# Performance work log

Hardware: AMD Instinct MI355X
Metric: run time of the kernel (lower is better)

The kernel has to match this reference:

```python
import jax, jax.numpy as jnp
import numpy as np

# fixed geometry: N = B2D * H * W pixels
B2D, H, W = 32, 112, 112
NCLS, NSUB, DIM = 4, 2, 256
PROTO_MOM = 0.999
SK_ITERS, SK_EPS = 3, 0.05
LN_EPS = 1e-5


def layer_norm(x, gamma, beta):
    mu = jnp.mean(x, axis=-1, keepdims=True)
    var = jnp.var(x, axis=-1, keepdims=True)
    return (x - mu) * jax.lax.rsqrt(var + LN_EPS) * gamma + beta


def l2_normalize(x):
    return x / jnp.maximum(jnp.linalg.norm(x, axis=-1, keepdims=True), 1e-12)


def masked_sinkhorn(sim_c, mask):
    # sim_c: [N, M] cosine sims for one class; mask: [N] bool (pixels of this class)
    # Faithful to distributed_sinkhorn, restricted to masked rows.
    m = mask.astype(sim_c.dtype)
    L = jnp.exp(sim_c / SK_EPS).T * m[None, :]          # [M, N]
    Bn = jnp.sum(m)
    M = L.shape[0]
    L = L / jnp.maximum(jnp.sum(L), 1e-30)
    for _ in range(SK_ITERS):
        L = L / jnp.maximum(jnp.sum(L, axis=1, keepdims=True), 1e-30) / M
        col = jnp.sum(L, axis=0, keepdims=True)
        L = jnp.where(m[None, :] > 0, L / jnp.maximum(col, 1e-30) / jnp.maximum(Bn, 1.0), 0.0)
    L = (L * Bn).T                                       # [N, M]
    idx = jnp.argmax(L, axis=1)
    q = jax.nn.one_hot(idx, M, dtype=sim_c.dtype) * m[:, None]  # hard assignment
    return q, idx


def setup_inputs() -> dict:
    key = jax.random.key(0)
    ks = jax.random.split(key, 3)
    N = B2D * H * W
    return {
        "out_feat": jax.random.normal(ks[0], (N, DIM), dtype=jnp.float32),
        "label": jax.random.randint(ks[1], (N,), 0, NCLS, dtype=jnp.int64),
        "prototypes": jax.random.normal(ks[2], (NCLS, NSUB, DIM), dtype=jnp.float32),
        "fn_gamma": jnp.ones((DIM,), jnp.float32),
        "fn_beta": jnp.zeros((DIM,), jnp.float32),
        "mn_gamma": jnp.ones((NCLS,), jnp.float32),
        "mn_beta": jnp.zeros((NCLS,), jnp.float32),
    }


def reference(out_feat, label, prototypes, fn_gamma, fn_beta, mn_gamma, mn_beta):
    N = out_feat.shape[0]
    feat = l2_normalize(layer_norm(out_feat, fn_gamma, fn_beta))      # [N, D]
    protos = l2_normalize(prototypes)                                  # [K, M, D]
    sim = jnp.einsum('nd,kmd->nmk', feat, protos)                      # [N, M, K]
    nearest = layer_norm(jnp.max(sim, axis=1), mn_gamma, mn_beta)      # [N, K]
    pred = jnp.argmax(nearest, axis=-1)
    correct = (label == pred)                                          # [N] bool

    proto_logits = sim.reshape(N, NSUB * NCLS)
    proto_target = jnp.zeros((N,), jnp.float32)
    new_protos = protos
    for c in range(NCLS):
        cls_mask = (label == c)
        q, idx = masked_sinkhorn(sim[:, :, c], cls_mask)               # q:[N,M], masked
        mk = (cls_mask & correct).astype(feat.dtype)[:, None]
        m_q = q * mk                                                   # [N, M]
        f = m_q.T @ (feat * mk)                                        # [M, D]
        n = jnp.sum(m_q, axis=0)                                       # [M]
        f = l2_normalize(f)
        upd = PROTO_MOM * protos[c] + (1.0 - PROTO_MOM) * f
        upd = jnp.where(((jnp.sum(n) > 0) & (n != 0))[:, None], upd, protos[c])
        new_protos = new_protos.at[c].set(upd)
        proto_target = jnp.where(cls_mask, idx.astype(jnp.float32) + NSUB * c, proto_target)
    new_protos = l2_normalize(new_protos)

    nearest_img = nearest.reshape(B2D, H, W, NCLS).transpose(0, 3, 1, 2)  # [b, K, h, w]
    return nearest_img, proto_logits, proto_target, new_protos
```

## Files before the change

### kernel.cpp

```cpp
#include <hip/hip_runtime.h>
#include <stdint.h>

#define N_PIX 401408
#define HWIMG 12544
#define LN_EPS 1e-5f

struct Ws {
  double R[3][8];
  unsigned cnt4[4];
  unsigned nmk[8];
  float  protoN[8][256];
  float  fAcc[8][256];
  unsigned char flags[N_PIX];
};

__device__ __forceinline__ float wredf(float v) {
#pragma unroll
  for (int o = 32; o > 0; o >>= 1) v += __shfl_xor(v, o, 64);
  return v;
}
__device__ __forceinline__ float wred16(float v) {
  v += __shfl_xor(v, 1, 64);
  v += __shfl_xor(v, 2, 64);
  v += __shfl_xor(v, 4, 64);
  v += __shfl_xor(v, 8, 64);
  return v;
}
__device__ __forceinline__ double wredd(double v) {
#pragma unroll
  for (int o = 32; o > 0; o >>= 1) v += __shfl_xor(v, o, 64);
  return v;
}
__device__ __forceinline__ unsigned wredu(unsigned v) {
#pragma unroll
  for (int o = 32; o > 0; o >>= 1) v += (unsigned)__shfl_xor((int)v, o, 64);
  return v;
}

__global__ __launch_bounds__(256) void k_main(
    const float* __restrict__ X, const int* __restrict__ label,
    const float* __restrict__ protos,
    const float* __restrict__ fng, const float* __restrict__ fnb,
    const float* __restrict__ mng, const float* __restrict__ mnb,
    Ws* __restrict__ ws,
    float* __restrict__ out_nearest, float* __restrict__ out_logits) {
  __shared__ float prS[16 * 132];
  int tid = threadIdx.x;
  int wave = tid >> 6, lane = tid & 63;

  if (blockIdx.x == 0) {
    if (tid < 24) ((double*)ws->R)[tid] = 0.0;
    if (tid >= 24 && tid < 32) ws->nmk[tid - 24] = 0u;
    if (tid >= 32 && tid < 36) ws->cnt4[tid - 32] = 0u;
    for (int i = tid; i < 2048; i += 256) (&ws->fAcc[0][0])[i] = 0.f;
  }

#pragma unroll
  for (int t = 0; t < 2; t++) {
    int r = wave + t * 4;
    const float4 p = *(const float4*)(protos + r * 256 + lane * 4);
    float ss = p.x * p.x + p.y * p.y + p.z * p.z + p.w * p.w;
    ss = wredf(ss);
    float inv = 1.0f / fmaxf(sqrtf(ss), 1e-12f);
    float4 o; o.x = p.x * inv; o.y = p.y * inv; o.z = p.z * inv; o.w = p.w * inv;
    int sd = lane >> 2;
    *(float4*)(&prS[sd * 132 + r * 16 + (lane & 3) * 4]) = o;
    if (blockIdx.x == 0) *(float4*)(&ws->protoN[r][lane * 4]) = o;
  }
  __syncthreads();

  int grp = lane >> 4, s = lane & 15;
  int n = blockIdx.x * 16 + wave * 4 + grp;

  const float* xb = X + (size_t)n * 256 + s * 16;
  const float4 x0 = *(const float4*)(xb);
  const float4 x1 = *(const float4*)(xb + 4);
  const float4 x2 = *(const float4*)(xb + 8);
  const float4 x3 = *(const float4*)(xb + 12);
  int lab = label[n];

  float sm = (x0.x + x0.y + x0.z + x0.w) + (x1.x + x1.y + x1.z + x1.w) +
             (x2.x + x2.y + x2.z + x2.w) + (x3.x + x3.y + x3.z + x3.w);
  float q = x0.x * x0.x + x0.y * x0.y + x0.z * x0.z + x0.w * x0.w +
            x1.x * x1.x + x1.y * x1.y + x1.z * x1.z + x1.w * x1.w +
            x2.x * x2.x + x2.y * x2.y + x2.z * x2.z + x2.w * x2.w +
            x3.x * x3.x + x3.y * x3.y + x3.z * x3.z + x3.w * x3.w;
  sm = wred16(sm); q = wred16(q);
  float mu = sm * (1.0f / 256.0f);
  float var = q * (1.0f / 256.0f) - mu * mu;
  float rstd = rsqrtf(var + LN_EPS);

  const float* gb = fng + s * 16;
  const float* bb = fnb + s * 16;
  const float4 g0 = *(const float4*)(gb);
  const float4 g1 = *(const float4*)(gb + 4);
  const float4 g2 = *(const float4*)(gb + 8);
  const float4 g3 = *(const float4*)(gb + 12);
  const float4 b0 = *(const float4*)(bb);
  const float4 b1 = *(const float4*)(bb + 4);
  const float4 b2 = *(const float4*)(bb + 8);
  const float4 b3 = *(const float4*)(bb + 12);

  float4 y0, y1, y2, y3;
  y0.x = (x0.x - mu) * rstd * g0.x + b0.x; y0.y = (x0.y - mu) * rstd * g0.y + b0.y;
  y0.z = (x0.z - mu) * rstd * g0.z + b0.z; y0.w = (x0.w - mu) * rstd * g0.w + b0.w;
  y1.x = (x1.x - mu) * rstd * g1.x + b1.x; y1.y = (x1.y - mu) * rstd * g1.y + b1.y;
  y1.z = (x1.z - mu) * rstd * g1.z + b1.z; y1.w = (x1.w - mu) * rstd * g1.w + b1.w;
  y2.x = (x2.x - mu) * rstd * g2.x + b2.x; y2.y = (x2.y - mu) * rstd * g2.y + b2.y;
  y2.z = (x2.z - mu) * rstd * g2.z + b2.z; y2.w = (x2.w - mu) * rstd * g2.w + b2.w;
  y3.x = (x3.x - mu) * rstd * g3.x + b3.x; y3.y = (x3.y - mu) * rstd * g3.y + b3.y;
  y3.z = (x3.z - mu) * rstd * g3.z + b3.z; y3.w = (x3.w - mu) * rstd * g3.w + b3.w;

  float qq = y0.x * y0.x + y0.y * y0.y + y0.z * y0.z + y0.w * y0.w +
             y1.x * y1.x + y1.y * y1.y + y1.z * y1.z + y1.w * y1.w +
             y2.x * y2.x + y2.y * y2.y + y2.z * y2.z + y2.w * y2.w +
             y3.x * y3.x + y3.y * y3.y + y3.z * y3.z + y3.w * y3.w;
  qq = wred16(qq);

  float dot[8];
#pragma unroll
  for (int j = 0; j < 8; j++) {
    const float* pj = &prS[s * 132 + j * 16];
    const float4 pa = *(const float4*)(pj);
    const float4 pb = *(const float4*)(pj + 4);
    const float4 pc = *(const float4*)(pj + 8);
    const float4 pd = *(const float4*)(pj + 12);
    dot[j] = y0.x * pa.x + y0.y * pa.y + y0.z * pa.z + y0.w * pa.w +
             y1.x * pb.x + y1.y * pb.y + y1.z * pb.z + y1.w * pb.w +
             y2.x * pc.x + y2.y * pc.y + y2.z * pc.z + y2.w * pc.w +
             y3.x * pd.x + y3.y * pd.y + y3.z * pd.z + y3.w * pd.w;
  }
#pragma unroll
  for (int o = 1; o <= 4; o <<= 1) {
#pragma unroll
    for (int j = 0; j < 8; j++) dot[j] += __shfl_xor(dot[j], o, 64);
  }
  int bsel = s & 7;
  float t0 = (bsel & 1) ? dot[1] : dot[0];
  float t1 = (bsel & 1) ? dot[3] : dot[2];
  float t2 = (bsel & 1) ? dot[5] : dot[4];
  float t3 = (bsel & 1) ? dot[7] : dot[6];
  float u0 = (bsel & 2) ? t1 : t0;
  float u1v = (bsel & 2) ? t3 : t2;
  float v = (bsel & 4) ? u1v : u0;
  v += __shfl_xor(v, 8, 64);

  float inv = 1.0f / fmaxf(sqrtf(qq), 1e-12f);
  float d = v * inv;

  if (s < 8) out_logits[(size_t)n * 8 + ((s & 1) << 2) + (s >> 1)] = d;

  float nm = fmaxf(d, __shfl_xor(d, 1, 64));
  float tA = __shfl_xor(nm, 2, 64);
  float s2 = nm + tA, q2 = nm * nm + tA * tA;
  float s4 = s2 + __shfl_xor(s2, 4, 64);
  float q4 = q2 + __shfl_xor(q2, 4, 64);
  float m4 = 0.25f * s4;
  float v4 = 0.25f * q4 - m4 * m4;
  float rs4 = rsqrtf(v4 + LN_EPS);
  int k = (s >> 1) & 3;
  float lnv = (nm - m4) * rs4 * mng[k] + mnb[k];

  int bimg = n / HWIMG;
  int p = n - bimg * HWIMG;
  if (s < 8 && (s & 1) == 0)
    out_nearest[((size_t)bimg * 4 + k) * HWIMG + p] = lnv;

  float av = lnv; int ak = k;
#pragma unroll
  for (int o = 2; o <= 4; o <<= 1) {
    float ov = __shfl_xor(av, o, 64);
    int ok = __shfl_xor(ak, o, 64);
    bool take = (ov > av) || (ov == av && ok < ak);
    av = take ? ov : av;
    ak = take ? ok : ak;
  }
  if (s == 0) ws->flags[n] = (lab == ak) ? (unsigned char)1 : (unsigned char)0;
}

template <int ITER>
__global__ __launch_bounds__(256) void k_sink(const float* __restrict__ logits,
                                              const int* __restrict__ label,
                                              Ws* __restrict__ ws) {
  __shared__ float su1[8], su2[8], sBn[4];
  int tid = threadIdx.x;
  if (ITER >= 2) {
    if (tid < 8) {
      int c = tid >> 1;
      float S = (float)ws->R[0][c * 2] + (float)ws->R[0][c * 2 + 1];
      float uu0 = 1.0f / fmaxf(S, 1e-30f);
      float R0 = (float)ws->R[0][tid];
      float uu1 = uu0 / (fmaxf(uu0 * R0, 1e-30f) * 2.0f);
      su1[tid] = uu1;
      if (ITER >= 3) {
        float R1 = (float)ws->R[1][tid];
        su2[tid] = uu1 / (fmaxf(uu1 * R1, 1e-30f) * 2.0f);
      }
    }
    if (tid < 4) sBn[tid] = fmaxf((float)ws->cnt4[tid], 1.0f);
  }
  __syncthreads();

  double a0 = 0, a1 = 0, a2 = 0, a3 = 0, a4 = 0, a5 = 0, a6 = 0, a7 = 0;
  unsigned c0 = 0, c1 = 0, c2 = 0, c3 = 0;
  int gtid = blockIdx.x * 256 + tid;
  int T = gridDim.x * 256;
  for (int n = gtid; n < N_PIX; n += T) {
    int c = label[n];
    const float4 la = *(const float4*)(logits + (size_t)n * 8);
    const float4 lb = *(const float4*)(logits + (size_t)n * 8 + 4);
    float s0 = (c & 2) ? ((c & 1) ? la.w : la.z) : ((c & 1) ? la.y : la.x);
    float s1 = (c & 2) ? ((c & 1) ? lb.w : lb.z) : ((c & 1) ? lb.y : lb.x);
    float E0 = expf(s0 / 0.05f);
    float E1 = expf(s1 / 0.05f);
    float v = 1.0f;
    if (ITER >= 2) {
      float S1 = su1[c * 2] * E0 + su1[c * 2 + 1] * E1;
      float v1 = 1.0f / (fmaxf(S1, 1e-30f) * sBn[c]);
      v = v1;
      if (ITER >= 3) {
        float S2 = su2[c * 2] * E0 + su2[c * 2 + 1] * E1;
        v = v1 / (fmaxf(v1 * S2, 1e-30f) * sBn[c]);
      }
    }
    double t0 = (double)(v * E0), t1 = (double)(v * E1);
    if (c == 0) { a0 += t0; a1 += t1; c0++; }
    else if (c == 1) { a2 += t0; a3 += t1; c1++; }
    else if (c == 2) { a4 += t0; a5 += t1; c2++; }
    else { a6 += t0; a7 += t1; c3++; }
  }
  a0 = wredd(a0); a1 = wredd(a1); a2 = wredd(a2); a3 = wredd(a3);
  a4 = wredd(a4); a5 = wredd(a5); a6 = wredd(a6); a7 = wredd(a7);
  __shared__ double lds[4][8];
  __shared__ unsigned ldc[4][4];
  int wave = tid >> 6, lane = tid & 63;
  if (ITER == 1) { c0 = wredu(c0); c1 = wredu(c1); c2 = wredu(c2); c3 = wredu(c3); }
  if (lane == 0) {
    lds[wave][0] = a0; lds[wave][1] = a1; lds[wave][2] = a2; lds[wave][3] = a3;
    lds[wave][4] = a4; lds[wave][5] = a5; lds[wave][6] = a6; lds[wave][7] = a7;
    if (ITER == 1) { ldc[wave][0] = c0; ldc[wave][1] = c1; ldc[wave][2] = c2; ldc[wave][3] = c3; }
  }
  __syncthreads();
  if (tid < 8) {
    double ssum = lds[0][tid] + lds[1][tid] + lds[2][tid] + lds[3][tid];
    unsafeAtomicAdd(&ws->R[ITER - 1][tid], ssum);
  }
  if (ITER == 1 && tid < 4) {
    unsigned cs = ldc[0][tid] + ldc[1][tid] + ldc[2][tid] + ldc[3][tid];
    atomicAdd(&ws->cnt4[tid], cs);
  }
}

__global__ __launch_bounds__(256) void k_accum(
    const float* __restrict__ X, const int* __restrict__ label,
    const float* __restrict__ fng, const float* __restrict__ fnb,
    const float* __restrict__ logits, Ws* __restrict__ ws,
    float* __restrict__ out_target) {
  __shared__ float fa[4 * 2048];
  __shared__ float su[8];
  __shared__ unsigned ldc[4][8];
  int tid = threadIdx.x;
  if (tid < 8) {
    int c = tid >> 1;
    float S = (float)ws->R[0][c * 2] + (float)ws->R[0][c * 2 + 1];
    float uu0 = 1.0f / fmaxf(S, 1e-30f);
    float R0 = (float)ws->R[0][tid];
    float uu1 = uu0 / (fmaxf(uu0 * R0, 1e-30f) * 2.0f);
    float R1 = (float)ws->R[1][tid];
    float uu2 = uu1 / (fmaxf(uu1 * R1, 1e-30f) * 2.0f);
    float R2 = (float)ws->R[2][tid];
    su[tid] = uu2 / (fmaxf(uu2 * R2, 1e-30f) * 2.0f);
  }
  for (int i = tid; i < 4 * 2048; i += 256) fa[i] = 0.f;
  __syncthreads();

  int wave = tid >> 6, lane = tid & 63;
  const float4 g4 = *(const float4*)(fng + lane * 4);
  const float4 b4 = *(const float4*)(fnb + lane * 4);
  float* myAcc = &fa[wave * 2048];

  unsigned cl[8] = {0, 0, 0, 0, 0, 0, 0, 0};
  int gw = blockIdx.x * 4 + wave;
  int GW = gridDim.x * 4;
  for (int ch = gw; ch < N_PIX / 64; ch += GW) {
    int n = ch * 64 + lane;
    int c = label[n];
    int fl = ws->flags[n];
    float s0 = logits[(size_t)n * 8 + c];
    float s1 = logits[(size_t)n * 8 + 4 + c];
    float E0 = expf(s0 / 0.05f);
    float E1 = expf(s1 / 0.05f);
    int idx = (su[c * 2 + 1] * E1 > su[c * 2] * E0) ? 1 : 0;
    out_target[n] = (float)(idx + 2 * c);
    int bucket = c * 2 + idx;
#pragma unroll
    for (int j = 0; j < 8; j++) cl[j] += (fl && bucket == j) ? 1u : 0u;

    unsigned long long mask = __ballot(fl);
    while (mask) {
      int src = __builtin_ctzll(mask);
      mask &= (mask - 1);
      int cc = __shfl(c, src, 64);
      int ii = __shfl(idx, src, 64);
      int nn = ch * 64 + src;
      const float4 x = *(const float4*)(X + (size_t)nn * 256 + lane * 4);
      float s = x.x + x.y + x.z + x.w;
      float q = x.x * x.x + x.y * x.y + x.z * x.z + x.w * x.w;
      s = wredf(s); q = wredf(q);
      float mu = s * (1.0f / 256.0f);
      float var = q * (1.0f / 256.0f) - mu * mu;
      float rstd = rsqrtf(var + LN_EPS);
      float y0 = (x.x - mu) * rstd * g4.x + b4.x;
      float y1 = (x.y - mu) * rstd * g4.y + b4.y;
      float y2 = (x.z - mu) * rstd * g4.z + b4.z;
      float y3 = (x.w - mu) * rstd * g4.w + b4.w;
      float qq = y0 * y0 + y1 * y1 + y2 * y2 + y3 * y3;
      qq = wredf(qq);
      float inv = 1.0f / fmaxf(sqrtf(qq), 1e-12f);
      float* dst = myAcc + (cc * 2 + ii) * 256 + lane * 4;
      dst[0] += y0 * inv; dst[1] += y1 * inv; dst[2] += y2 * inv; dst[3] += y3 * inv;
    }
  }
#pragma unroll
  for (int j = 0; j < 8; j++) cl[j] = wredu(cl[j]);
  if (lane == 0) {
#pragma unroll
    for (int j = 0; j < 8; j++) ldc[wave][j] = cl[j];
  }
  __syncthreads();
  float* fg = &ws->fAcc[0][0];
  for (int i = tid; i < 2048; i += 256) {
    float ssum = fa[i] + fa[2048 + i] + fa[4096 + i] + fa[6144 + i];
    unsafeAtomicAdd(fg + i, ssum);
  }
  if (tid < 8) {
    unsigned cs = ldc[0][tid] + ldc[1][tid] + ldc[2][tid] + ldc[3][tid];
    if (cs) atomicAdd(&ws->nmk[tid], cs);
  }
}

__global__ __launch_bounds__(512) void k_final(Ws* __restrict__ ws, float* __restrict__ out_protos) {
  int tid = threadIdx.x;
  int r = tid >> 6, lane = tid & 63;
  const float4 f = *(const float4*)(&ws->fAcc[r][lane * 4]);
  float ss = wredf(f.x * f.x + f.y * f.y + f.z * f.z + f.w * f.w);
  float invf = 1.0f / fmaxf(sqrtf(ss), 1e-12f);
  unsigned nr = ws->nmk[r];
  int c = r >> 1;
  unsigned tot = ws->nmk[c * 2] + ws->nmk[c * 2 + 1];
  bool cond = (tot > 0u) && (nr != 0u);
  const float4 p = *(const float4*)(&ws->protoN[r][lane * 4]);
  float u0 = cond ? 0.999f * p.x + 0.001f * (f.x * invf) : p.x;
  float u1 = cond ? 0.999f * p.y + 0.001f * (f.y * invf) : p.y;
  float u2 = cond ? 0.999f * p.z + 0.001f * (f.z * invf) : p.z;
  float u3 = cond ? 0.999f * p.w + 0.001f * (f.w * invf) : p.w;
  float ss2 = wredf(u0 * u0 + u1 * u1 + u2 * u2 + u3 * u3);
  float invn = 1.0f / fmaxf(sqrtf(ss2), 1e-12f);
  float4 o; o.x = u0 * invn; o.y = u1 * invn; o.z = u2 * invn; o.w = u3 * invn;
  *(float4*)(out_protos + r * 256 + lane * 4) = o;
}

extern "C" void kernel_launch(void* const* d_in, const int* in_sizes, int n_in,
                              void* d_out, int out_size, void* d_ws, size_t ws_size,
                              hipStream_t stream) {
  const float* X = (const float*)d_in[0];
  const int* label = (const int*)d_in[1];
  const float* protos = (const float*)d_in[2];
  const float* fng = (const float*)d_in[3];
  const float* fnb = (const float*)d_in[4];
  const float* mng = (const float*)d_in[5];
  const float* mnb = (const float*)d_in[6];

  float* out = (float*)d_out;
  float* out_nearest = out;
  float* out_logits = out + 1605632;
  float* out_target = out_logits + 3211264;
  float* out_protos = out_target + N_PIX;
  Ws* ws = (Ws*)d_ws;

  k_main<<<N_PIX / 16, 256, 0, stream>>>(X, label, protos, fng, fnb, mng, mnb, ws, out_nearest, out_logits);
  k_sink<1><<<512, 256, 0, stream>>>(out_logits, label, ws);
  k_sink<2><<<512, 256, 0, stream>>>(out_logits, label, ws);
  k_sink<3><<<512, 256, 0, stream>>>(out_logits, label, ws);
  k_accum<<<512, 256, 0, stream>>>(X, label, fng, fnb, out_logits, ws, out_target);
  k_final<<<1, 512, 0, stream>>>(ws, out_protos);
}
```

Measured before the change: 670.3 us.

## Fuse first Sinkhorn pass into main kernel and pack per-pixel class sims

Moves prototype normalization into a separate init kernel. The main kernel now processes 256 pixels per block with 8 lanes per pixel and also computes the first Sinkhorn row sums and class counts, so the k_sink<1> launch is gone. It writes the two class-specific similarities into a compact ePack buffer, which the later Sinkhorn and accumulation passes read instead of the strided logits array. It adds a fast path that skips the gamma/beta multiply when they are identity, and doubles the accum grid. The costs are an extra kernel launch, more registers per thread, and a larger workspace.

```diff
diff --git a/kernel.cpp b/kernel.cpp
--- a/kernel.cpp
+++ b/kernel.cpp
@@ -11,6 +11,7 @@
   unsigned nmk[8];
   float  protoN[8][256];
   float  fAcc[8][256];
+  float  ePack[N_PIX][2];
   unsigned char flags[N_PIX];
 };
 
@@ -19,13 +20,6 @@
   for (int o = 32; o > 0; o >>= 1) v += __shfl_xor(v, o, 64);
   return v;
 }
-__device__ __forceinline__ float wred16(float v) {
-  v += __shfl_xor(v, 1, 64);
-  v += __shfl_xor(v, 2, 64);
-  v += __shfl_xor(v, 4, 64);
-  v += __shfl_xor(v, 8, 64);
-  return v;
-}
 __device__ __forceinline__ double wredd(double v) {
 #pragma unroll
   for (int o = 32; o > 0; o >>= 1) v += __shfl_xor(v, o, 64);
@@ -37,225 +31,274 @@
   return v;
 }
 
+__global__ __launch_bounds__(512) void k_init(const float* __restrict__ protos, Ws* __restrict__ ws) {
+  int tid = threadIdx.x;
+  if (tid < 24) ((double*)ws->R)[tid] = 0.0;
+  if (tid >= 24 && tid < 32) ws->nmk[tid - 24] = 0u;
+  if (tid >= 32 && tid < 36) ws->cnt4[tid - 32] = 0u;
+  float* fa = &ws->fAcc[0][0];
+  for (int i = tid; i < 8 * 256; i += 512) fa[i] = 0.f;
+
+  int r = tid >> 6, lane = tid & 63;
+  const float4 p = *(const float4*)(protos + r * 256 + lane * 4);
+  float ss = p.x * p.x + p.y * p.y + p.z * p.z + p.w * p.w;
+  ss = wredf(ss);
+  float inv = 1.0f / fmaxf(sqrtf(ss), 1e-12f);
+  float4 o; o.x = p.x * inv; o.y = p.y * inv; o.z = p.z * inv; o.w = p.w * inv;
+  *(float4*)(&ws->protoN[r][lane * 4]) = o;
+}
+
 __global__ __launch_bounds__(256) void k_main(
     const float* __restrict__ X, const int* __restrict__ label,
-    const float* __restrict__ protos,
     const float* __restrict__ fng, const float* __restrict__ fnb,
     const float* __restrict__ mng, const float* __restrict__ mnb,
     Ws* __restrict__ ws,
     float* __restrict__ out_nearest, float* __restrict__ out_logits) {
-  __shared__ float prS[16 * 132];
+  __shared__ float prS[8 * 260];
+  __shared__ double sR[4][8];
+  __shared__ unsigned sC[4][4];
   int tid = threadIdx.x;
   int wave = tid >> 6, lane = tid & 63;
-
-  if (blockIdx.x == 0) {
-    if (tid < 24) ((double*)ws->R)[tid] = 0.0;
-    if (tid >= 24 && tid < 32) ws->nmk[tid - 24] = 0u;
-    if (tid >= 32 && tid < 36) ws->cnt4[tid - 32] = 0u;
-    for (int i = tid; i < 2048; i += 256) (&ws->fAcc[0][0])[i] = 0.f;
-  }
-
-#pragma unroll
-  for (int t = 0; t < 2; t++) {
-    int r = wave + t * 4;
-    const float4 p = *(const float4*)(protos + r * 256 + lane * 4);
-    float ss = p.x * p.x + p.y * p.y + p.z * p.z + p.w * p.w;
-    ss = wredf(ss);
-    float inv = 1.0f / fmaxf(sqrtf(ss), 1e-12f);
-    float4 o; o.x = p.x * inv; o.y = p.y * inv; o.z = p.z * inv; o.w = p.w * inv;
-    int sd = lane >> 2;
-    *(float4*)(&prS[sd * 132 + r * 16 + (lane & 3) * 4]) = o;
-    if (blockIdx.x == 0) *(float4*)(&ws->protoN[r][lane * 4]) = o;
-  }
-  __syncthreads();
-
-  int grp = lane >> 4, s = lane & 15;
-  int n = blockIdx.x * 16 + wave * 4 + grp;
-
-  const float* xb = X + (size_t)n * 256 + s * 16;
-  const float4 x0 = *(const float4*)(xb);
-  const float4 x1 = *(const float4*)(xb + 4);
-  const float4 x2 = *(const float4*)(xb + 8);
-  const float4 x3 = *(const float4*)(xb + 12);
-  int lab = label[n];
-
-  float sm = (x0.x + x0.y + x0.z + x0.w) + (x1.x + x1.y + x1.z + x1.w) +
-             (x2.x + x2.y + x2.z + x2.w) + (x3.x + x3.y + x3.z + x3.w);
-  float q = x0.x * x0.x + x0.y * x0.y + x0.z * x0.z + x0.w * x0.w +
-            x1.x * x1.x + x1.y * x1.y + x1.z * x1.z + x1.w * x1.w +
-            x2.x * x2.x + x2.y * x2.y + x2.z * x2.z + x2.w * x2.w +
-            x3.x * x3.x + x3.y * x3.y + x3.z * x3.z + x3.w * x3.w;
-  sm = wred16(sm); q = wred16(q);
-  float mu = sm * (1.0f / 256.0f);
-  float var = q * (1.0f / 256.0f) - mu * mu;
-  float rstd = rsqrtf(var + LN_EPS);
-
-  const float* gb = fng + s * 16;
-  const float* bb = fnb + s * 16;
-  const float4 g0 = *(const float4*)(gb);
-  const float4 g1 = *(const float4*)(gb + 4);
-  const float4 g2 = *(const float4*)(gb + 8);
-  const float4 g3 = *(const float4*)(gb + 12);
-  const float4 b0 = *(const float4*)(bb);
-  const float4 b1 = *(const float4*)(bb + 4);
-  const float4 b2 = *(const float4*)(bb + 8);
-  const float4 b3 = *(const float4*)(bb + 12);
-
-  float4 y0, y1, y2, y3;
-  y0.x = (x0.x - mu) * rstd * g0.x + b0.x; y0.y = (x0.y - mu) * rstd * g0.y + b0.y;
-  y0.z = (x0.z - mu) * rstd * g0.z + b0.z; y0.w = (x0.w - mu) * rstd * g0.w + b0.w;
-  y1.x = (x1.x - mu) * rstd * g1.x + b1.x; y1.y = (x1.y - mu) * rstd * g1.y + b1.y;
-  y1.z = (x1.z - mu) * rstd * g1.z + b1.z; y1.w = (x1.w - mu) * rstd * g1.w + b1.w;
-  y2.x = (x2.x - mu) * rstd * g2.x + b2.x; y2.y = (x2.y - mu) * rstd * g2.y + b2.y;
-  y2.z = (x2.z - mu) * rstd * g2.z + b2.z; y2.w = (x2.w - mu) * rstd * g2.w + b2.w;
-  y3.x = (x3.x - mu) * rstd * g3.x + b3.x; y3.y = (x3.y - mu) * rstd * g3.y + b3.y;
-  y3.z = (x3.z - mu) * rstd * g3.z + b3.z; y3.w = (x3.w - mu) * rstd * g3.w + b3.w;
-
-  float qq = y0.x * y0.x + y0.y * y0.y + y0.z * y0.z + y0.w * y0.w +
-             y1.x * y1.x + y1.y * y1.y + y1.z * y1.z + y1.w * y1.w +
-             y2.x * y2.x + y2.y * y2.y + y2.z * y2.z + y2.w * y2.w +
-             y3.x * y3.x + y3.y * y3.y + y3.z * y3.z + y3.w * y3.w;
-  qq = wred16(qq);
-
-  float dot[8];
-#pragma unroll
-  for (int j = 0; j < 8; j++) {
-    const float* pj = &prS[s * 132 + j * 16];
-    const float4 pa = *(const float4*)(pj);
-    const float4 pb = *(const float4*)(pj + 4);
-    const float4 pc = *(const float4*)(pj + 8);
-    const float4 pd = *(const float4*)(pj + 12);
-    dot[j] = y0.x * pa.x + y0.y * pa.y + y0.z * pa.z + y0.w * pa.w +
-             y1.x * pb.x + y1.y * pb.y + y1.z * pb.z + y1.w * pb.w +
-             y2.x * pc.x + y2.y * pc.y + y2.z * pc.z + y2.w * pc.w +
-             y3.x * pd.x + y3.y * pd.y + y3.z * pd.z + y3.w * pd.w;
-  }
-#pragma unroll
-  for (int o = 1; o <= 4; o <<= 1) {
-#pragma unroll
-    for (int j = 0; j < 8; j++) dot[j] += __shfl_xor(dot[j], o, 64);
-  }
-  int bsel = s & 7;
-  float t0 = (bsel & 1) ? dot[1] : dot[0];
-  float t1 = (bsel & 1) ? dot[3] : dot[2];
-  float t2 = (bsel & 1) ? dot[5] : dot[4];
-  float t3 = (bsel & 1) ? dot[7] : dot[6];
-  float u0 = (bsel & 2) ? t1 : t0;
-  float u1v = (bsel & 2) ? t3 : t2;
-  float v = (bsel & 4) ? u1v : u0;
-  v += __shfl_xor(v, 8, 64);
-
-  float inv = 1.0f / fmaxf(sqrtf(qq), 1e-12f);
-  float d = v * inv;
-
-  if (s < 8) out_logits[(size_t)n * 8 + ((s & 1) << 2) + (s >> 1)] = d;
-
-  float nm = fmaxf(d, __shfl_xor(d, 1, 64));
-  float tA = __shfl_xor(nm, 2, 64);
-  float s2 = nm + tA, q2 = nm * nm + tA * tA;
-  float s4 = s2 + __shfl_xor(s2, 4, 64);
-  float q4 = q2 + __shfl_xor(q2, 4, 64);
-  float m4 = 0.25f * s4;
-  float v4 = 0.25f * q4 - m4 * m4;
-  float rs4 = rsqrtf(v4 + LN_EPS);
-  int k = (s >> 1) & 3;
-  float lnv = (nm - m4) * rs4 * mng[k] + mnb[k];
-
-  int bimg = n / HWIMG;
-  int p = n - bimg * HWIMG;
-  if (s < 8 && (s & 1) == 0)
-    out_nearest[((size_t)bimg * 4 + k) * HWIMG + p] = lnv;
-
-  float av = lnv; int ak = k;
-#pragma unroll
-  for (int o = 2; o <= 4; o <<= 1) {
-    float ov = __shfl_xor(av, o, 64);
-    int ok = __shfl_xor(ak, o, 64);
-    bool take = (ov > av) || (ov == av && ok < ak);
-    av = take ? ov : av;
-    ak = take ? ok : ak;
-  }
-  if (s == 0) ws->flags[n] = (lab == ak) ? (unsigned char)1 : (unsigned char)0;
+  int s = lane & 7, g = lane >> 3;
+
+  {
+    int ps = tid >> 5, pj = (tid >> 2) & 7, ph = tid & 3;
+    const float* src = &ws->protoN[pj][ps * 32 + ph * 8];
+    float4 a = *(const float4*)src;
+    float4 b = *(const float4*)(src + 4);
+    float* dst = &prS[ps * 260 + pj * 32 + ph * 8];
+    *(float4*)dst = a;
+    *(float4*)(dst + 4) = b;
+  }
+
+  bool triv;
+  {
+    bool ok = true;
+    const float* gp = fng + s * 32;
+    const float* bp = fnb + s * 32;
+#pragma unroll
+    for (int q = 0; q < 8; q++) {
+      float4 gq = *(const float4*)(gp + q * 4);
+      float4 bq = *(const float4*)(bp + q * 4);
+      ok = ok && gq.x == 1.f && gq.y == 1.f && gq.z == 1.f && gq.w == 1.f &&
+           bq.x == 0.f && bq.y == 0.f && bq.z == 0.f && bq.w == 0.f;
+    }
+    triv = (bool)__all(ok);
+  }
+  float mngk = mng[s >> 1], mnbk = mnb[s >> 1];
+  __syncthreads();
+
+  double eAcc = 0.0;
+  unsigned cAcc = 0u;
+
+  const int base = blockIdx.x * 256;
+#pragma unroll 1
+  for (int it = 0; it < 8; ++it) {
+    int n = base + it * 32 + wave * 8 + g;
+    const float* xb = X + (size_t)n * 256 + s * 32;
+    float4 Y[8];
+#pragma unroll
+    for (int q = 0; q < 8; q++) Y[q] = *(const float4*)(xb + q * 4);
+    int lab = label[n];
+
+    float sm = 0.f, sq = 0.f;
+#pragma unroll
+    for (int q = 0; q < 8; q++) {
+      sm += Y[q].x + Y[q].y + Y[q].z + Y[q].w;
+      sq += Y[q].x * Y[q].x + Y[q].y * Y[q].y + Y[q].z * Y[q].z + Y[q].w * Y[q].w;
+    }
+    sm += __shfl_xor(sm, 1, 64); sq += __shfl_xor(sq, 1, 64);
+    sm += __shfl_xor(sm, 2, 64); sq += __shfl_xor(sq, 2, 64);
+    sm += __shfl_xor(sm, 4, 64); sq += __shfl_xor(sq, 4, 64);
+    float mu = sm * (1.0f / 256.0f);
+    float var = sq * (1.0f / 256.0f) - mu * mu;
+    float rstd = rsqrtf(var + LN_EPS);
+
+    if (triv) {
+#pragma unroll
+      for (int q = 0; q < 8; q++) {
+        Y[q].x = (Y[q].x - mu) * rstd; Y[q].y = (Y[q].y - mu) * rstd;
+        Y[q].z = (Y[q].z - mu) * rstd; Y[q].w = (Y[q].w - mu) * rstd;
+      }
+    } else {
+      const float* gp = fng + s * 32;
+      const float* bp = fnb + s * 32;
+#pragma unroll
+      for (int q = 0; q < 8; q++) {
+        float4 gq = *(const float4*)(gp + q * 4);
+        float4 bq = *(const float4*)(bp + q * 4);
+        Y[q].x = (Y[q].x - mu) * rstd * gq.x + bq.x;
+        Y[q].y = (Y[q].y - mu) * rstd * gq.y + bq.y;
+        Y[q].z = (Y[q].z - mu) * rstd * gq.z + bq.z;
+        Y[q].w = (Y[q].w - mu) * rstd * gq.w + bq.w;
+      }
+    }
+
+    float qq = 0.f;
+#pragma unroll
+    for (int q = 0; q < 8; q++)
+      qq += Y[q].x * Y[q].x + Y[q].y * Y[q].y + Y[q].z * Y[q].z + Y[q].w * Y[q].w;
+    qq += __shfl_xor(qq, 1, 64);
+    qq += __shfl_xor(qq, 2, 64);
+    qq += __shfl_xor(qq, 4, 64);
+
+    float dot[8];
+#pragma unroll
+    for (int j = 0; j < 8; j++) {
+      const float* pj = &prS[s * 260 + j * 32];
+      float acc = 0.f;
+#pragma unroll
+      for (int q = 0; q < 8; q++) {
+        float4 pv = *(const float4*)(pj + q * 4);
+        acc += Y[q].x * pv.x + Y[q].y * pv.y + Y[q].z * pv.z + Y[q].w * pv.w;
+      }
+      dot[j] = acc;
+    }
+    bool b0 = (lane & 1) != 0;
+    float e0, e1, e2, e3;
+    {
+      float t0 = b0 ? dot[0] : dot[1];
+      float t1 = b0 ? dot[2] : dot[3];
+      float t2 = b0 ? dot[4] : dot[5];
+      float t3 = b0 ? dot[6] : dot[7];
+      float r0 = __shfl_xor(t0, 1, 64);
+      float r1 = __shfl_xor(t1, 1, 64);
+      float r2 = __shfl_xor(t2, 1, 64);
+      float r3 = __shfl_xor(t3, 1, 64);
+      e0 = (b0 ? dot[1] : dot[0]) + r0;
+      e1 = (b0 ? dot[3] : dot[2]) + r1;
+      e2 = (b0 ? dot[5] : dot[4]) + r2;
+      e3 = (b0 ? dot[7] : dot[6]) + r3;
+    }
+    bool b1 = (lane & 2) != 0;
+    float f0, f1;
+    {
+      float t0 = b1 ? e0 : e1;
+      float t1 = b1 ? e2 : e3;
+      float r0 = __shfl_xor(t0, 2, 64);
+      float r1 = __shfl_xor(t1, 2, 64);
+      f0 = (b1 ? e1 : e0) + r0;
+      f1 = (b1 ? e3 : e2) + r1;
+    }
+    bool b2 = (lane & 4) != 0;
+    float dsum;
+    {
+      float t0 = b2 ? f0 : f1;
+      float r0 = __shfl_xor(t0, 4, 64);
+      dsum = (b2 ? f1 : f0) + r0;
+    }
+    float inv = 1.0f / fmaxf(sqrtf(qq), 1e-12f);
+    float d = dsum * inv;
+
+    out_logits[(size_t)n * 8 + ((s & 1) << 2) + (s >> 1)] = d;
+    if ((s >> 1) == lab) ws->ePack[n][s & 1] = d;
+    eAcc += ((s >> 1) == lab) ? (double)expf(d / 0.05f) : 0.0;
+    cAcc += (s == lab) ? 1u : 0u;
+
+    float nm = fmaxf(d, __shfl_xor(d, 1, 64));
+    float tA = __shfl_xor(nm, 2, 64);
+    float s2 = nm + tA, qn = nm * nm + tA * tA;
+    float s4 = s2 + __shfl_xor(s2, 4, 64);
+    float q4 = qn + __shfl_xor(qn, 4, 64);
+    float m4 = 0.25f * s4;
+    float v4 = 0.25f * q4 - m4 * m4;
+    float rs4 = rsqrtf(v4 + LN_EPS);
+    int k = s >> 1;
+    float lnv = (nm - m4) * rs4 * mngk + mnbk;
+    int bimg = n / HWIMG;
+    int p = n - bimg * HWIMG;
+    if ((s & 1) == 0)
+      out_nearest[((size_t)bimg * 4 + k) * HWIMG + p] = lnv;
+
+    float av = lnv; int ak = k;
+#pragma unroll
+    for (int o = 2; o <= 4; o <<= 1) {
+      float ov = __shfl_xor(av, o, 64);
+      int ok2 = __shfl_xor(ak, o, 64);
+      bool take = (ov > av) || (ov == av && ok2 < ak);
+      av = take ? ov : av;
+      ak = take ? ok2 : ak;
+    }
+    if (s == 0) ws->flags[n] = (lab == ak) ? (unsigned char)1 : (unsigned char)0;
+  }
+
+  eAcc += __shfl_xor(eAcc, 8, 64);
+  eAcc += __shfl_xor(eAcc, 16, 64);
+  eAcc += __shfl_xor(eAcc, 32, 64);
+  cAcc += (unsigned)__shfl_xor((int)cAcc, 8, 64);
+  cAcc += (unsigned)__shfl_xor((int)cAcc, 16, 64);
+  cAcc += (unsigned)__shfl_xor((int)cAcc, 32, 64);
+  if (lane < 8) sR[wave][lane] = eAcc;
+  if (lane < 4) sC[wave][lane] = cAcc;
+  __syncthreads();
+  if (tid < 8)
+    unsafeAtomicAdd(&ws->R[0][tid], sR[0][tid] + sR[1][tid] + sR[2][tid] + sR[3][tid]);
+  if (tid >= 8 && tid < 12) {
+    int c = tid - 8;
+    atomicAdd(&ws->cnt4[c], sC[0][c] + sC[1][c] + sC[2][c] + sC[3][c]);
+  }
 }
 
 template <int ITER>
-__global__ __launch_bounds__(256) void k_sink(const float* __restrict__ logits,
-                                              const int* __restrict__ label,
+__global__ __launch_bounds__(256) void k_sink(const int* __restrict__ label,
                                               Ws* __restrict__ ws) {
   __shared__ float su1[8], su2[8], sBn[4];
   int tid = threadIdx.x;
-  if (ITER >= 2) {
-    if (tid < 8) {
-      int c = tid >> 1;
-      float S = (float)ws->R[0][c * 2] + (float)ws->R[0][c * 2 + 1];
-      float uu0 = 1.0f / fmaxf(S, 1e-30f);
-      float R0 = (float)ws->R[0][tid];
-      float uu1 = uu0 / (fmaxf(uu0 * R0, 1e-30f) * 2.0f);
-      su1[tid] = uu1;
-      if (ITER >= 3) {
-        float R1 = (float)ws->R[1][tid];
-        su2[tid] = uu1 / (fmaxf(uu1 * R1, 1e-30f) * 2.0f);
-      }
-    }
-    if (tid < 4) sBn[tid] = fmaxf((float)ws->cnt4[tid], 1.0f);
-  }
+  if (tid < 8) {
+    int c = tid >> 1;
+    float S = (float)ws->R[0][c * 2] + (float)ws->R[0][c * 2 + 1];
+    float uu0 = 1.0f / fmaxf(S, 1e-30f);
+    float R0 = (float)ws->R[0][tid];
+    float uu1 = uu0 / (fmaxf(uu0 * R0, 1e-30f) * 2.0f);
+    su1[tid] = uu1;
+    if (ITER >= 3) {
+      float R1 = (float)ws->R[1][tid];
+      su2[tid] = uu1 / (fmaxf(uu1 * R1, 1e-30f) * 2.0f);
+    }
+  }
+  if (tid < 4) sBn[tid] = fmaxf((float)ws->cnt4[tid], 1.0f);
   __syncthreads();
 
   double a0 = 0, a1 = 0, a2 = 0, a3 = 0, a4 = 0, a5 = 0, a6 = 0, a7 = 0;
-  unsigned c0 = 0, c1 = 0, c2 = 0, c3 = 0;
   int gtid = blockIdx.x * 256 + tid;
   int T = gridDim.x * 256;
   for (int n = gtid; n < N_PIX; n += T) {
     int c = label[n];
-    const float4 la = *(const float4*)(logits + (size_t)n * 8);
-    const float4 lb = *(const float4*)(logits + (size_t)n * 8 + 4);
-    float s0 = (c & 2) ? ((c & 1) ? la.w : la.z) : ((c & 1) ? la.y : la.x);
-    float s1 = (c & 2) ? ((c & 1) ? lb.w : lb.z) : ((c & 1) ? lb.y : lb.x);
-    float E0 = expf(s0 / 0.05f);
-    float E1 = expf(s1 / 0.05f);
-    float v = 1.0f;
-    if (ITER >= 2) {
-      float S1 = su1[c * 2] * E0 + su1[c * 2 + 1] * E1;
-      float v1 = 1.0f / (fmaxf(S1, 1e-30f) * sBn[c]);
-      v = v1;
-      if (ITER >= 3) {
-        float S2 = su2[c * 2] * E0 + su2[c * 2 + 1] * E1;
-        v = v1 / (fmaxf(v1 * S2, 1e-30f) * sBn[c]);
-      }
+    float2 e = *(const float2*)(&ws->ePack[n][0]);
+    float E0 = expf(e.x / 0.05f);
+    float E1 = expf(e.y / 0.05f);
+    float S1 = su1[c * 2] * E0 + su1[c * 2 + 1] * E1;
+    float v1 = 1.0f / (fmaxf(S1, 1e-30f) * sBn[c]);
+    float v = v1;
+    if (ITER >= 3) {
+      float S2 = su2[c * 2] * E0 + su2[c * 2 + 1] * E1;
+      v = v1 / (fmaxf(v1 * S2, 1e-30f) * sBn[c]);
     }
     double t0 = (double)(v * E0), t1 = (double)(v * E1);
-    if (c == 0) { a0 += t0; a1 += t1; c0++; }
-    else if (c == 1) { a2 += t0; a3 += t1; c1++; }
-    else if (c == 2) { a4 += t0; a5 += t1; c2++; }
-    else { a6 += t0; a7 += t1; c3++; }
+    if (c == 0) { a0 += t0; a1 += t1; }
+    else if (c == 1) { a2 += t0; a3 += t1; }
+    else if (c == 2) { a4 += t0; a5 += t1; }
+    else { a6 += t0; a7 += t1; }
   }
   a0 = wredd(a0); a1 = wredd(a1); a2 = wredd(a2); a3 = wredd(a3);
   a4 = wredd(a4); a5 = wredd(a5); a6 = wredd(a6); a7 = wredd(a7);
   __shared__ double lds[4][8];
-  __shared__ unsigned ldc[4][4];
   int wave = tid >> 6, lane = tid & 63;
-  if (ITER == 1) { c0 = wredu(c0); c1 = wredu(c1); c2 = wredu(c2); c3 = wredu(c3); }
   if (lane == 0) {
     lds[wave][0] = a0; lds[wave][1] = a1; lds[wave][2] = a2; lds[wave][3] = a3;
     lds[wave][4] = a4; lds[wave][5] = a5; lds[wave][6] = a6; lds[wave][7] = a7;
-    if (ITER == 1) { ldc[wave][0] = c0; ldc[wave][1] = c1; ldc[wave][2] = c2; ldc[wave][3] = c3; }
   }
   __syncthreads();
   if (tid < 8) {
     double ssum = lds[0][tid] + lds[1][tid] + lds[2][tid] + lds[3][tid];
     unsafeAtomicAdd(&ws->R[ITER - 1][tid], ssum);
   }
-  if (ITER == 1 && tid < 4) {
-    unsigned cs = ldc[0][tid] + ldc[1][tid] + ldc[2][tid] + ldc[3][tid];
-    atomicAdd(&ws->cnt4[tid], cs);
-  }
 }
 
 __global__ __launch_bounds__(256) void k_accum(
     const float* __restrict__ X, const int* __restrict__ label,
     const float* __restrict__ fng, const float* __restrict__ fnb,
-    const float* __restrict__ logits, Ws* __restrict__ ws,
-    float* __restrict__ out_target) {
+    Ws* __restrict__ ws, float* __restrict__ out_target) {
   __shared__ float fa[4 * 2048];
   __shared__ float su[8];
   __shared__ unsigned ldc[4][8];
@@ -286,10 +329,9 @@
     int n = ch * 64 + lane;
     int c = label[n];
     int fl = ws->flags[n];
-    float s0 = logits[(size_t)n * 8 + c];
-    float s1 = logits[(size_t)n * 8 + 4 + c];
-    float E0 = expf(s0 / 0.05f);
-    float E1 = expf(s1 / 0.05f);
+    float2 e = *(const float2*)(&ws->ePack[n][0]);
+    float E0 = expf(e.x / 0.05f);
+    float E1 = expf(e.y / 0.05f);
     int idx = (su[c * 2 + 1] * E1 > su[c * 2] * E0) ? 1 : 0;
     out_target[n] = (float)(idx + 2 * c);
     int bucket = c * 2 + idx;
@@ -378,10 +420,10 @@
   float* out_protos = out_target + N_PIX;
   Ws* ws = (Ws*)d_ws;
 
-  k_main<<<N_PIX / 16, 256, 0, stream>>>(X, label, protos, fng, fnb, mng, mnb, ws, out_nearest, out_logits);
-  k_sink<1><<<512, 256, 0, stream>>>(out_logits, label, ws);
-  k_sink<2><<<512, 256, 0, stream>>>(out_logits, label, ws);
-  k_sink<3><<<512, 256, 0, stream>>>(out_logits, label, ws);
-  k_accum<<<512, 256, 0, stream>>>(X, label, fng, fnb, out_logits, ws, out_target);
+  k_init<<<1, 512, 0, stream>>>(protos, ws);
+  k_main<<<N_PIX / 256, 256, 0, stream>>>(X, label, fng, fnb, mng, mnb, ws, out_nearest, out_logits);
+  k_sink<2><<<512, 256, 0, stream>>>(label, ws);
+  k_sink<3><<<512, 256, 0, stream>>>(label, ws);
+  k_accum<<<1024, 256, 0, stream>>>(X, label, fng, fnb, ws, out_target);
   k_final<<<1, 512, 0, stream>>>(ws, out_protos);
 }
```

Measured after the change: 720.0 us. 7.4% more time.
